# Performance work log

Measured on AMD Instinct MI355X. Metric: run time of the kernel, lower is better.

The kernel has to match this reference:

```python
import jax, jax.numpy as jnp
import numpy as np

B, T, Rn, D, O, E, H, C, TM = 20, 20, 20, 4096, 16, 512, 8, 68, 1900


def l2norm(x, axis=-1, eps=1e-12):
    return x / jnp.maximum(jnp.linalg.norm(x, axis=axis, keepdims=True), eps)


def setup_inputs() -> dict:
    key = jax.random.key(0)
    ks = jax.random.split(key, 10)
    return {
        "features": jax.random.normal(ks[0], (B, T, Rn, D), jnp.float32),
        "labels": jax.random.randint(ks[1], (B, O), 0, C),
        "temporal_mem": jax.random.normal(ks[2], (TM, T, D), jnp.float32),
        "entity_W": jax.random.normal(ks[3], (C, E), jnp.float32) / np.float32(np.sqrt(C)),
        "entity_b": jnp.zeros((E,), jnp.float32),
        "Wq": jax.random.normal(ks[4], (E, E), jnp.float32) / np.float32(np.sqrt(E)),
        "Wk": jax.random.normal(ks[5], (D, E), jnp.float32) / np.float32(np.sqrt(D)),
        "Wv": jax.random.normal(ks[6], (D, E), jnp.float32) / np.float32(np.sqrt(D)),
        "Wo": jax.random.normal(ks[7], (E, E), jnp.float32) / np.float32(np.sqrt(E)),
        "obj_W1": jax.random.normal(ks[8], (D, E), jnp.float32) / np.float32(np.sqrt(D)),
        "obj_b1": jnp.zeros((E,), jnp.float32),
        "obj_W2": jax.random.normal(ks[9], (E, 1), jnp.float32) / np.float32(np.sqrt(E)),
        "obj_b2": jnp.zeros((1,), jnp.float32),
    }


def reference(features, labels, temporal_mem, entity_W, entity_b, Wq, Wk, Wv, Wo,
              obj_W1, obj_b1, obj_W2, obj_b2):
    beta = 0.5   # loss mixing weight (module's beta)
    qgce = 0.7   # generalized-CE exponent
    Dh = E // H
    # region features, L2-normalized (dataset_feat == 'CVPR' path)
    Rf = l2norm(features)                                   # [B,T,Rn,D]

    # ---- temporal memory-bank kNN retrieval ----
    R_max = l2norm(jnp.max(Rf, axis=2))                     # [B,T,D] max-pool over regions
    mem_max = l2norm(jnp.max(temporal_mem, axis=1))         # [TM,D] max-pool over frames
    sim = jnp.einsum('btd,md->btm', R_max, mem_max)         # [B,T,TM]
    idx = jnp.argmax(sim, axis=-1)                          # [B,T] nearest memory slot
    Rp = temporal_mem[idx]                                  # [B,T,T,D] gathered memory videos
    mem_feat = jnp.max(Rp, axis=2)                          # [B,T,D]

    # ---- entity (object-label) embedding: one-hot with class 0 zeroed ----
    onehot = jax.nn.one_hot(labels, C, dtype=features.dtype)
    onehot = onehot * (labels != 0)[..., None].astype(features.dtype)
    Qe = onehot @ entity_W + entity_b                       # [B,O,E]

    # ---- multi-head attention fusion over regions + retrieved memory ----
    kv = jnp.concatenate([Rf.reshape(B, T * Rn, D), mem_feat], axis=1)  # [B,N,D]
    q = (Qe @ Wq).reshape(B, O, H, Dh)
    k = (kv @ Wk).reshape(B, -1, H, Dh)
    v = (kv @ Wv).reshape(B, -1, H, Dh)
    scores = jnp.einsum('bohd,bnhd->bhon', q, k) / np.float32(np.sqrt(Dh))
    attn = jax.nn.softmax(scores, axis=-1)
    fused = jnp.einsum('bhon,bnhd->bohd', attn, v).reshape(B, O, E) @ Wo  # [B,O,E]

    # ---- top-k region objectness selection + generalized CE ----
    QR = jax.lax.stop_gradient(jnp.mean(scores, axis=1)[:, :, :T * Rn].reshape(B, O, T, Rn))
    hi = jnp.argmax(QR, axis=-1)                            # [B,O,T] top-1 region
    lo = jnp.argmin(QR, axis=-1)                            # [B,O,T] low region
    bidx = jnp.arange(B)[:, None, None]
    tidx = jnp.arange(T)[None, None, :]
    R_high = Rf[bidx, tidx, hi]                             # [B,O,T,D]
    R_low = Rf[bidx, tidx, lo]                              # [B,O,T,D]
    osel = (labels != 0).astype(features.dtype)             # [B,O]
    onum = jnp.maximum(jnp.sum(osel, axis=1), 1.0)
    mlp = lambda x: jax.nn.sigmoid(jnp.tanh(x @ obj_W1 + obj_b1) @ obj_W2 + obj_b2)
    s_hi = mlp(R_high * osel[..., None, None]).squeeze(-1)  # [B,O,T]
    s_lo = mlp(R_low * osel[..., None, None]).squeeze(-1)
    gce_hi = jnp.mean((1.0 - (s_hi + 1e-7) ** qgce) / qgce * osel[..., None], axis=-1)
    gce_lo = jnp.mean((1.0 - (1.0 - s_lo + 1e-7) ** qgce) / qgce * osel[..., None], axis=-1)
    gce = jnp.mean(jnp.sum(gce_hi, axis=1) / onum) + jnp.mean(jnp.sum(gce_lo, axis=1) / onum)

    return fused + beta * gce
```

## Files before the change

### kernel.cpp

```cpp
#include <hip/hip_runtime.h>

#define B_   20
#define T_   20
#define RN   20
#define D_   4096
#define O_   16
#define E_   512
#define H_   8
#define DH   64
#define TM_  1900
#define MREG 8192
#define NW   1536
#define NSIM 2048
#define MSIM 512
#define CAP  256

using f32x4  = __attribute__((ext_vector_type(4))) float;
using bf16x8 = __attribute__((ext_vector_type(8))) __bf16;

__device__ __forceinline__ unsigned short f2bf(float f){
  unsigned u = __float_as_uint(f);
  u += 0x7fffu + ((u >> 16) & 1u);
  return (unsigned short)(u >> 16);
}

__device__ __forceinline__ void st_bf4(unsigned short* dst, float4 v){
  ushort4 o = make_ushort4(f2bf(v.x), f2bf(v.y), f2bf(v.z), f2bf(v.w));
  *(ushort4*)dst = o;
}

__device__ __forceinline__ float bsum256(float v, float* sh){
  int t = threadIdx.x;
  for (int o = 32; o; o >>= 1) v += __shfl_down(v, o, 64);
  __syncthreads();
  if ((t & 63) == 0) sh[t >> 6] = v;
  __syncthreads();
  return sh[0] + sh[1] + sh[2] + sh[3];
}

__device__ __forceinline__ float bmax256(float v, float* sh){
  int t = threadIdx.x;
  for (int o = 32; o; o >>= 1) v = fmaxf(v, __shfl_down(v, o, 64));
  __syncthreads();
  if ((t & 63) == 0) sh[t >> 6] = v;
  __syncthreads();
  return fmaxf(fmaxf(sh[0], sh[1]), fmaxf(sh[2], sh[3]));
}

__device__ __forceinline__ void gld16(const void* g, void* l){
  __builtin_amdgcn_global_load_lds(
      (const __attribute__((address_space(1))) unsigned int*)g,
      (__attribute__((address_space(3))) unsigned int*)l, 16, 0, 0);
}

__global__ __launch_bounds__(256) void k_pre(
    const float* __restrict__ F, const float* __restrict__ TMm,
    const float* __restrict__ Wk, const float* __restrict__ Wv, const float* __restrict__ W1,
    unsigned short* __restrict__ Wall,
    unsigned short* __restrict__ A, float* __restrict__ rmaxr, float* __restrict__ rmsum,
    unsigned short* __restrict__ ubf,
    float* __restrict__ umax, float* __restrict__ msum, unsigned short* __restrict__ wnorm,
    unsigned short* __restrict__ gbf,
    const int* __restrict__ labels, const float* __restrict__ entW, const float* __restrict__ entB,
    const float* __restrict__ Wq, float* __restrict__ q){
  __shared__ char smem[4352];
  int bid = blockIdx.x, t = threadIdx.x;
  if (bid < 2048){
    int m = bid;
    if (m >= TM_){
      int4 zz = make_int4(0,0,0,0);
      int4* r1 = (int4*)(wnorm + (size_t)m*D_);
      int4* r2 = (int4*)(gbf + (size_t)m*D_);
      r1[t] = zz; r1[t + 256] = zz;
      r2[t] = zz; r2[t + 256] = zz;
      return;
    }
    float* sh = (float*)smem;
    const float* base = TMm + (size_t)m*T_*D_;
    float4 mx[4];
#pragma unroll
    for (int i = 0; i < 4; ++i) mx[i] = make_float4(-1e30f,-1e30f,-1e30f,-1e30f);
    for (int f = 0; f < T_; ++f){
#pragma unroll
      for (int i = 0; i < 4; ++i){
        float4 v = *(const float4*)(base + (size_t)f*D_ + i*1024 + t*4);
        mx[i].x = fmaxf(mx[i].x, v.x); mx[i].y = fmaxf(mx[i].y, v.y);
        mx[i].z = fmaxf(mx[i].z, v.z); mx[i].w = fmaxf(mx[i].w, v.w);
      }
    }
    float s = 0.f;
#pragma unroll
    for (int i = 0; i < 4; ++i){
      *(float4*)(umax + (size_t)m*D_ + i*1024 + t*4) = mx[i];
      st_bf4(gbf + (size_t)m*D_ + i*1024 + t*4, mx[i]);
      s += mx[i].x*mx[i].x + mx[i].y*mx[i].y + mx[i].z*mx[i].z + mx[i].w*mx[i].w;
    }
    s = bsum256(s, sh);
    if (t == 0) msum[m] = s;
    float inv = 1.f / fmaxf(sqrtf(s), 1e-12f);
#pragma unroll
    for (int i = 0; i < 4; ++i){
      float4 u = mx[i];
      u.x *= inv; u.y *= inv; u.z *= inv; u.w *= inv;
      st_bf4(wnorm + (size_t)m*D_ + i*1024 + t*4, u);
    }
  } else if (bid < 2560){
    int bt = bid - 2048;
    if (bt >= 400){
      int4 zz = make_int4(0,0,0,0);
      int4* r1 = (int4*)(ubf + (size_t)bt*D_);
      r1[t] = zz; r1[t + 256] = zz;
      int base = 8000 + (bt - 400)*2;
#pragma unroll
      for (int k = 0; k < 2; ++k){
        if (base + k < MREG){
          int4* r2 = (int4*)(A + (size_t)(base + k)*D_);
          r2[t] = zz; r2[t + 256] = zz;
        }
      }
      return;
    }
    float* sh = (float*)smem;
    const float* fb = F + (size_t)bt*RN*D_;
    unsigned short* ab = A + (size_t)bt*RN*D_;
    float4 mx[4];
#pragma unroll
    for (int i = 0; i < 4; ++i) mx[i] = make_float4(-1e30f,-1e30f,-1e30f,-1e30f);
    float4 vn[4];
#pragma unroll
    for (int i = 0; i < 4; ++i) vn[i] = *(const float4*)(fb + i*1024 + t*4);
    for (int r = 0; r < RN; ++r){
      float4 v[4];
      float s = 0.f;
#pragma unroll
      for (int i = 0; i < 4; ++i){
        v[i] = vn[i];
        s += v[i].x*v[i].x + v[i].y*v[i].y + v[i].z*v[i].z + v[i].w*v[i].w;
      }
      if (r + 1 < RN){
#pragma unroll
        for (int i = 0; i < 4; ++i)
          vn[i] = *(const float4*)(fb + (size_t)(r+1)*D_ + i*1024 + t*4);
      }
      s = bsum256(s, sh);
      float ri = 1.f / fmaxf(sqrtf(s), 1e-12f);
#pragma unroll
      for (int i = 0; i < 4; ++i){
        v[i].x *= ri; v[i].y *= ri; v[i].z *= ri; v[i].w *= ri;
        st_bf4(ab + (size_t)r*D_ + i*1024 + t*4, v[i]);
        mx[i].x = fmaxf(mx[i].x, v[i].x); mx[i].y = fmaxf(mx[i].y, v[i].y);
        mx[i].z = fmaxf(mx[i].z, v[i].z); mx[i].w = fmaxf(mx[i].w, v[i].w);
      }
    }
    float s2 = 0.f;
#pragma unroll
    for (int i = 0; i < 4; ++i){
      *(float4*)(rmaxr + (size_t)bt*D_ + i*1024 + t*4) = mx[i];
      s2 += mx[i].x*mx[i].x + mx[i].y*mx[i].y + mx[i].z*mx[i].z + mx[i].w*mx[i].w;
    }
    s2 = bsum256(s2, sh);
    if (t == 0) rmsum[bt] = s2;
    float inv = 1.f / fmaxf(sqrtf(s2), 1e-12f);
#pragma unroll
    for (int i = 0; i < 4; ++i){
      float4 u = mx[i];
      u.x *= inv; u.y *= inv; u.z *= inv; u.w *= inv;
      st_bf4(ubf + (size_t)bt*D_ + i*1024 + t*4, u);
    }
  } else if (bid < 8704){
    int wti = bid - 2560;
    float* tile = (float*)smem;
    int kb = (wti & 127) * 32, nb = (wti >> 7) * 32;
    const float* src; int nc0;
    if (nb < 512)      { src = Wk; nc0 = nb; }
    else if (nb < 1024){ src = Wv; nc0 = nb - 512; }
    else               { src = W1; nc0 = nb - 1024; }
    int tx = t & 31, ty = t >> 5;
#pragma unroll
    for (int j = 0; j < 4; ++j){
      int k = kb + ty + j*8;
      tile[(ty + j*8)*33 + tx] = src[(size_t)k*E_ + nc0 + tx];
    }
    __syncthreads();
#pragma unroll
    for (int j = 0; j < 4; ++j){
      int n = nb + ty + j*8;
      int k = kb + tx;
      Wall[(size_t)n*D_ + k] = f2bf(tile[tx*33 + ty + j*8]);
    }
  } else {
    int bo = bid - 8704;
    float* qe = (float*)smem;
    int lab = labels[bo];
    float sel = (lab != 0) ? 1.f : 0.f;
    qe[t]       = sel * entW[(size_t)lab*E_ + t]       + entB[t];
    qe[t + 256] = sel * entW[(size_t)lab*E_ + t + 256] + entB[t + 256];
    __syncthreads();
    float a0 = 0.f, a1 = 0.f;
    for (int ep = 0; ep < E_; ++ep){
      float r = qe[ep];
      a0 += r * Wq[(size_t)ep*E_ + t];
      a1 += r * Wq[(size_t)ep*E_ + t + 256];
    }
    q[(size_t)bo*E_ + t] = a0;
    q[(size_t)bo*E_ + t + 256] = a1;
  }
}

__global__ __launch_bounds__(512, 1) void k_gemm3(
    const unsigned short* __restrict__ Akv, const unsigned short* __restrict__ Wall,
    const unsigned short* __restrict__ ubf, const unsigned short* __restrict__ wnorm,
    const unsigned short* __restrict__ gbf,
    float* __restrict__ C2, float* __restrict__ simc, float* __restrict__ Gc){
  __shared__ char lds[131072];
  int bid = blockIdx.x;
  bid = (bid & 7)*32 + (bid >> 3);
  const unsigned short *A, *Bw; float* C; int nNt, ldc, mt, nt;
  if (bid < 192){       A = Akv; Bw = Wall;  C = C2;   nNt = 6; ldc = NW;   mt = bid/6;  nt = bid%6; }
  else if (bid < 208){  int s = bid - 192;
                        A = ubf; Bw = wnorm; C = simc; nNt = 8; ldc = NSIM; mt = s/8;    nt = s%8; }
  else {                int s = bid - 208;
                        A = gbf; Bw = Wall;  C = Gc;   nNt = 6; ldc = NW;   mt = s/6;    nt = s%6; }
  int tid = threadIdx.x, wid = tid >> 6, l = tid & 63;
  int wr = (wid >> 2) * 128;
  int wc = (wid & 3) * 64;
  int fr = l & 15, fq = l >> 4;
  const char* Ab = (const char*)A + (size_t)mt*256*(size_t)(D_*2);
  const char* Bb = (const char*)Bw + (size_t)nt*256*(size_t)(D_*2);
  f32x4 acc[8][4];
#pragma unroll
  for (int m = 0; m < 8; ++m)
#pragma unroll
    for (int n = 0; n < 4; ++n) acc[m][n] = (f32x4){0.f,0.f,0.f,0.f};

#pragma unroll
  for (int i = 0; i < 4; ++i){
    int idx = i*512 + tid;
    int row = idx >> 3, u = idx & 7;
    int ul = u ^ (row & 7);
    gld16(Ab + (size_t)row*(D_*2) + (size_t)(ul*16), lds + idx*16);
    gld16(Bb + (size_t)row*(D_*2) + (size_t)(ul*16), lds + 32768 + idx*16);
  }
  __syncthreads();

  int c = 0;
  for (int kt = 0; kt < D_/64; ++kt){
    if (kt < D_/64 - 1){
      int ktoff = (kt + 1) * 128;
      char* dA = lds + (c^1)*65536;
      char* dB = dA + 32768;
#pragma unroll
      for (int i = 0; i < 4; ++i){
        int idx = i*512 + tid;
        int row = idx >> 3, u = idx & 7;
        int ul = u ^ (row & 7);
        gld16(Ab + (size_t)row*(D_*2) + ktoff + ul*16, dA + idx*16);
        gld16(Bb + (size_t)row*(D_*2) + ktoff + ul*16, dB + idx*16);
      }
    }
    const char* LA = lds + c*65536;
    const char* LB = LA + 32768;
    bf16x8 bv[4][2];
#pragma unroll
    for (int n = 0; n < 4; ++n)
#pragma unroll
      for (int kk = 0; kk < 2; ++kk){
        int row = wc + n*16 + fr;
        int u = (kk*4 + fq) ^ (row & 7);
        bv[n][kk] = *(const bf16x8*)(LB + row*128 + u*16);
      }
    __builtin_amdgcn_s_setprio(1);
#pragma unroll
    for (int mp = 0; mp < 4; ++mp){
      bf16x8 av[2][2];
#pragma unroll
      for (int mm = 0; mm < 2; ++mm)
#pragma unroll
        for (int kk = 0; kk < 2; ++kk){
          int row = wr + (mp*2 + mm)*16 + fr;
          int u = (kk*4 + fq) ^ (row & 7);
          av[mm][kk] = *(const bf16x8*)(LA + row*128 + u*16);
        }
#pragma unroll
      for (int mm = 0; mm < 2; ++mm)
#pragma unroll
        for (int n = 0; n < 4; ++n)
#pragma unroll
          for (int kk = 0; kk < 2; ++kk)
            acc[mp*2 + mm][n] = __builtin_amdgcn_mfma_f32_16x16x32_bf16(
                av[mm][kk], bv[n][kk], acc[mp*2 + mm][n], 0, 0, 0);
    }
    __builtin_amdgcn_s_setprio(0);
    __syncthreads();
    c ^= 1;
  }
  size_t crow0 = (size_t)mt*256 + wr, ccol0 = (size_t)nt*256 + wc;
#pragma unroll
  for (int m = 0; m < 8; ++m)
#pragma unroll
    for (int n = 0; n < 4; ++n){
      size_t r0 = crow0 + m*16 + fq*4, c0 = ccol0 + n*16 + fr;
#pragma unroll
      for (int j = 0; j < 4; ++j)
        C[(r0 + j)*(size_t)ldc + c0] = acc[m][n][j];
    }
}

__global__ __launch_bounds__(256) void k_pick(const float* __restrict__ simc,
                                              const float* __restrict__ rmaxr, const float* __restrict__ rmsum,
                                              const float* __restrict__ umax, const float* __restrict__ msum,
                                              const float* __restrict__ Gc, float* __restrict__ C2){
  int bt = blockIdx.x, t = threadIdx.x;
  __shared__ float srow[1920];
  __shared__ float sh[4];
  __shared__ int cnt;
  __shared__ int cl[CAP];
  for (int m = t; m < TM_; m += 256) srow[m] = simc[(size_t)bt*NSIM + m];
  if (t == 0) cnt = 0;
  __syncthreads();
  float mx = -1e30f;
  for (int m = t; m < TM_; m += 256) mx = fmaxf(mx, srow[m]);
  mx = bmax256(mx, sh);
  float thr = mx - 2.5e-4f;
  for (int m = t; m < TM_; m += 256){
    if (srow[m] >= thr){
      int p = atomicAdd(&cnt, 1);
      if (p < CAP) cl[p] = m;
    }
  }
  __syncthreads();
  int cn = cnt < CAP ? cnt : CAP;
  float rinvv = 1.f / fmaxf(sqrtf(rmsum[bt]), 1e-12f);
  const float* a = rmaxr + (size_t)bt*D_;
  float best = -1e30f; int bestm = 0x7fffffff;
  for (int ci = 0; ci < cn; ++ci){
    int m = cl[ci];
    const float* wrow = umax + (size_t)m*D_;
    float p = 0.f;
    for (int i = t*4; i < D_; i += 1024){
      float4 av = *(const float4*)(a + i);
      float4 wv = *(const float4*)(wrow + i);
      p += av.x*wv.x + av.y*wv.y + av.z*wv.z + av.w*wv.w;
    }
    p = bsum256(p, sh);
    float sim = p * rinvv * (1.f / fmaxf(sqrtf(msum[m]), 1e-12f));
    if (sim > best || (sim == best && m < bestm)){ best = sim; bestm = m; }
  }
  const float4* src = (const float4*)(Gc + (size_t)bestm*NW);
  float4* dst = (float4*)(C2 + (size_t)(MREG + bt)*NW);
  if (t < 128){ dst[t] = src[t]; dst[t + 128] = src[t + 128]; dst[t + 256] = src[t + 256]; }
}

__global__ __launch_bounds__(256) void k_post(const float* __restrict__ q, const float* __restrict__ c2,
                                              float* __restrict__ fpre, int* __restrict__ hi,
                                              int* __restrict__ lo, const float* __restrict__ b1,
                                              const float* __restrict__ W2, const float* __restrict__ b2,
                                              float* __restrict__ z){
  __shared__ char smem[58368];
  int bid = blockIdx.x, t = threadIdx.x;
  if (bid < 160){
    int b = bid >> 3, h = bid & 7;
    int w = t >> 6, l = t & 63;
    float* qhp = (float*)smem;
    float* kb  = (float*)(smem + 4160);
    float* sc  = (float*)(smem + 31460);
    for (int i = t; i < O_*DH; i += 256){
      int o = i >> 6, d = i & 63;
      qhp[o*65 + d] = q[((size_t)(b*O_ + o))*E_ + h*DH + d] * 0.125f;
    }
    __syncthreads();
    for (int c = 0; c < 4; ++c){
      for (int i = t; i < 105*DH; i += 256){
        int j = i >> 6, d = i & 63;
        int n = c*105 + j;
        size_t row = n < 400 ? (size_t)b*400 + n : (size_t)MREG + b*20 + (n - 400);
        kb[j*65 + d] = c2[row*NW + h*DH + d];
      }
      __syncthreads();
      for (int i = t; i < O_*105; i += 256){
        int o = i / 105, j = i % 105;
        float acc = 0.f;
        for (int d = 0; d < DH; ++d) acc += qhp[o*65 + d] * kb[j*65 + d];
        sc[o*420 + c*105 + j] = acc;
      }
      __syncthreads();
    }
    for (int oi = 0; oi < 4; ++oi){
      int o = w + oi*4;
      float mxv = -1e30f;
      for (int n = l; n < 420; n += 64) mxv = fmaxf(mxv, sc[o*420 + n]);
      for (int of = 32; of; of >>= 1) mxv = fmaxf(mxv, __shfl_xor(mxv, of, 64));
      float sum = 0.f;
      for (int n = l; n < 420; n += 64){ float e = expf(sc[o*420 + n] - mxv); sc[o*420 + n] = e; sum += e; }
      for (int of = 32; of; of >>= 1) sum += __shfl_xor(sum, of, 64);
      float inv = 1.f / sum;
      for (int n = l; n < 420; n += 64) sc[o*420 + n] *= inv;
    }
    __syncthreads();
    float acc[4] = {0.f, 0.f, 0.f, 0.f};
    for (int c = 0; c < 4; ++c){
      for (int i = t; i < 105*DH; i += 256){
        int j = i >> 6, d = i & 63;
        int n = c*105 + j;
        size_t row = n < 400 ? (size_t)b*400 + n : (size_t)MREG + b*20 + (n - 400);
        kb[j*65 + d] = c2[row*NW + E_ + h*DH + d];
      }
      __syncthreads();
#pragma unroll
      for (int og = 0; og < 4; ++og){
        int o = og*4 + w;
        float a = 0.f;
        for (int j = 0; j < 105; ++j) a += sc[o*420 + c*105 + j] * kb[j*65 + l];
        acc[og] += a;
      }
      __syncthreads();
    }
#pragma unroll
    for (int og = 0; og < 4; ++og){
      int o = og*4 + w;
      fpre[((size_t)(b*O_ + o))*E_ + h*DH + l] = acc[og];
    }
  } else if (bid < 560){
    int bt = bid - 160;
    int b = bt / T_, tt = bt % T_;
    float* kl = (float*)smem;
    float* qr = (float*)(smem + 41040);
    for (int i = t; i < RN*E_; i += 256){
      int r = i >> 9, e = i & 511;
      kl[r*513 + e] = c2[((size_t)b*400 + tt*RN + r)*NW + e];
    }
    __syncthreads();
#pragma unroll
    for (int pp = 0; pp < 2; ++pp){
      int p = t + pp*256;
      if (p < O_*RN){
        int o = p / RN, r = p % RN;
        const float* qrow = q + ((size_t)(b*O_ + o))*E_;
        float acc = 0.f;
        for (int e = 0; e < E_; ++e) acc += qrow[e] * kl[r*513 + e];
        qr[o*20 + r] = acc;
      }
    }
    __syncthreads();
    if (t < O_){
      int o = t;
      float bh = qr[o*20], bl = qr[o*20]; int ih = 0, il = 0;
#pragma unroll
      for (int r = 1; r < RN; ++r){
        float v = qr[o*20 + r];
        if (v > bh){ bh = v; ih = r; }
        if (v < bl){ bl = v; il = r; }
      }
      int rowbase = b*400 + tt*RN;
      int outi = (b*O_ + o)*T_ + tt;
      hi[outi] = rowbase + ih;
      lo[outi] = rowbase + il;
    }
  } else {
    int g = (bid - 560)*4 + (t >> 6);
    int l = t & 63;
    const float* hrow = c2 + (size_t)g*NW + 1024;
    float acc = 0.f;
    for (int e = l; e < E_; e += 64) acc += tanhf(hrow[e] + b1[e]) * W2[e];
    for (int of = 32; of; of >>= 1) acc += __shfl_down(acc, of, 64);
    if (l == 0) z[g] = 1.f / (1.f + expf(-(acc + b2[0])));
  }
}

__global__ __launch_bounds__(256) void k_outg(const float* __restrict__ fpre, const float* __restrict__ Wo,
                                              const float* __restrict__ z, const int* __restrict__ hi,
                                              const int* __restrict__ lo, const int* __restrict__ labels,
                                              float* __restrict__ out){
  int bo = blockIdx.x, t = threadIdx.x;
  __shared__ float rowv[E_];
  __shared__ float vb[B_];
  __shared__ int cb[B_];
  __shared__ float gsh;
  rowv[t] = fpre[(size_t)bo*E_ + t];
  rowv[t + 256] = fpre[(size_t)bo*E_ + t + 256];
  if (t < B_){ vb[t] = 0.f; cb[t] = 0; }
  __syncthreads();
  for (int p = t; p < B_*O_; p += 256){
    int b = p / O_;
    if (labels[p] != 0){
      float acc = 0.f;
      for (int tt = 0; tt < T_; ++tt){
        float shi = z[hi[p*T_ + tt]];
        float slo = z[lo[p*T_ + tt]];
        acc += (1.f - __powf(shi + 1e-7f, 0.7f)) / 0.7f;
        acc += (1.f - __powf(1.f - slo + 1e-7f, 0.7f)) / 0.7f;
      }
      atomicAdd(&vb[b], acc / (float)T_);
      atomicAdd(&cb[b], 1);
    }
  }
  __syncthreads();
  if (t == 0){
    float g = 0.f;
    for (int b = 0; b < B_; ++b) g += vb[b] / fmaxf((float)cb[b], 1.f);
    gsh = 0.5f * (g / (float)B_);
  }
  __syncthreads();
  float g = gsh;
  float a0 = 0.f, a1 = 0.f;
  for (int ep = 0; ep < E_; ++ep){
    float r = rowv[ep];
    a0 += r * Wo[(size_t)ep*E_ + t];
    a1 += r * Wo[(size_t)ep*E_ + t + 256];
  }
  out[(size_t)bo*E_ + t] = a0 + g;
  out[(size_t)bo*E_ + t + 256] = a1 + g;
}

extern "C" void kernel_launch(void* const* d_in, const int* in_sizes, int n_in,
                              void* d_out, int out_size, void* d_ws, size_t ws_size,
                              hipStream_t stream) {
  (void)in_sizes; (void)n_in; (void)out_size; (void)ws_size;
  const float* F    = (const float*)d_in[0];
  const int*   labels = (const int*)d_in[1];
  const float* TMm  = (const float*)d_in[2];
  const float* entW = (const float*)d_in[3];
  const float* entB = (const float*)d_in[4];
  const float* Wq   = (const float*)d_in[5];
  const float* Wk   = (const float*)d_in[6];
  const float* Wv   = (const float*)d_in[7];
  const float* Wo   = (const float*)d_in[8];
  const float* W1   = (const float*)d_in[9];
  const float* b1   = (const float*)d_in[10];
  const float* W2   = (const float*)d_in[11];
  const float* b2   = (const float*)d_in[12];
  float* out = (float*)d_out;

  size_t off = 0;
  char* wsb = (char*)d_ws;
  auto alloc = [&](size_t bytes) -> char* {
    char* p = wsb + off; off += (bytes + 255) & ~(size_t)255; return p;
  };
  unsigned short* A_kv = (unsigned short*)alloc((size_t)MREG * D_ * 2);
  unsigned short* Wall = (unsigned short*)alloc((size_t)NW * D_ * 2);
  float* umax          = (float*)alloc((size_t)TM_ * D_ * 4);
  unsigned short* gbf  = (unsigned short*)alloc((size_t)NSIM * D_ * 2);
  unsigned short* wnorm= (unsigned short*)alloc((size_t)NSIM * D_ * 2);
  unsigned short* ubf  = (unsigned short*)alloc((size_t)MSIM * D_ * 2);
  float* rmaxr = (float*)alloc((size_t)400 * D_ * 4);
  float* simc  = (float*)alloc((size_t)MSIM * NSIM * 4);
  float* Gc    = (float*)alloc((size_t)NSIM * NW * 4);
  float* C2    = (float*)alloc((size_t)(MREG + 512) * NW * 4);
  float* qbuf  = (float*)alloc((size_t)B_ * O_ * E_ * 4);
  float* fpre  = (float*)alloc((size_t)B_ * O_ * E_ * 4);
  float* rmsum = (float*)alloc(400 * 4);
  float* msum  = (float*)alloc(TM_ * 4);
  int*   hib   = (int*)alloc(6400 * 4);
  int*   lob   = (int*)alloc(6400 * 4);
  float* zbuf  = (float*)alloc(8000 * 4);

  k_pre<<<9024, 256, 0, stream>>>(F, TMm, Wk, Wv, W1, Wall, A_kv, rmaxr, rmsum, ubf,
                                  umax, msum, wnorm, gbf, labels, entW, entB, Wq, qbuf);
  k_gemm3<<<256, 512, 0, stream>>>(A_kv, Wall, ubf, wnorm, gbf, C2, simc, Gc);
  k_pick<<<400, 256, 0, stream>>>(simc, rmaxr, rmsum, umax, msum, Gc, C2);
  k_post<<<2560, 256, 0, stream>>>(qbuf, C2, fpre, hib, lob, b1, W2, b2, zbuf);
  k_outg<<<B_*O_, 256, 0, stream>>>(fpre, Wo, zbuf, hib, lob, labels, out);
}
```

Baseline: 485.9 us.

## Use triple-buffered K=32 LDS pipeline in GEMM and prefetch frames in max-pool

The main GEMM kernel moves from a double-buffered K=64 tile with full __syncthreads to a three-stage K=32 ring buffer. It uses explicit vmcnt waits and raw s_barrier so two tiles of global loads stay in flight while MFMAs run on the third. The LDS footprint drops from 128 KiB to 96 KiB and the swizzle changes to 4 chunks per row. The memory max-pool loop also double-buffers its frame loads in registers to hide load latency. The hand-written vmcnt counts depend on exactly four outstanding loads per stage, so any compiler reordering of those loads could make the waits insufficient.

```diff
diff --git a/kernel.cpp b/kernel.cpp
--- a/kernel.cpp
+++ b/kernel.cpp
@@ -14,6 +14,7 @@
 #define NSIM 2048
 #define MSIM 512
 #define CAP  256
+#define NT32 128
 
 using f32x4  = __attribute__((ext_vector_type(4))) float;
 using bf16x8 = __attribute__((ext_vector_type(8))) __bf16;
@@ -80,12 +81,21 @@
     float4 mx[4];
 #pragma unroll
     for (int i = 0; i < 4; ++i) mx[i] = make_float4(-1e30f,-1e30f,-1e30f,-1e30f);
+    float4 va[2][4];
+#pragma unroll
+    for (int i = 0; i < 4; ++i) va[0][i] = *(const float4*)(base + i*1024 + t*4);
+#pragma unroll
     for (int f = 0; f < T_; ++f){
+      int c = f & 1;
+      if (f + 1 < T_){
+#pragma unroll
+        for (int i = 0; i < 4; ++i)
+          va[c^1][i] = *(const float4*)(base + (size_t)(f+1)*D_ + i*1024 + t*4);
+      }
 #pragma unroll
       for (int i = 0; i < 4; ++i){
-        float4 v = *(const float4*)(base + (size_t)f*D_ + i*1024 + t*4);
-        mx[i].x = fmaxf(mx[i].x, v.x); mx[i].y = fmaxf(mx[i].y, v.y);
-        mx[i].z = fmaxf(mx[i].z, v.z); mx[i].w = fmaxf(mx[i].w, v.w);
+        mx[i].x = fmaxf(mx[i].x, va[c][i].x); mx[i].y = fmaxf(mx[i].y, va[c][i].y);
+        mx[i].z = fmaxf(mx[i].z, va[c][i].z); mx[i].w = fmaxf(mx[i].w, va[c][i].w);
       }
     }
     float s = 0.f;
@@ -212,7 +222,7 @@
     const unsigned short* __restrict__ ubf, const unsigned short* __restrict__ wnorm,
     const unsigned short* __restrict__ gbf,
     float* __restrict__ C2, float* __restrict__ simc, float* __restrict__ Gc){
-  __shared__ char lds[131072];
+  __shared__ char lds[98304];
   int bid = blockIdx.x;
   bid = (bid & 7)*32 + (bid >> 3);
   const unsigned short *A, *Bw; float* C; int nNt, ldc, mt, nt;
@@ -233,66 +243,60 @@
 #pragma unroll
     for (int n = 0; n < 4; ++n) acc[m][n] = (f32x4){0.f,0.f,0.f,0.f};
 
-#pragma unroll
-  for (int i = 0; i < 4; ++i){
-    int idx = i*512 + tid;
-    int row = idx >> 3, u = idx & 7;
-    int ul = u ^ (row & 7);
-    gld16(Ab + (size_t)row*(D_*2) + (size_t)(ul*16), lds + idx*16);
-    gld16(Bb + (size_t)row*(D_*2) + (size_t)(ul*16), lds + 32768 + idx*16);
-  }
-  __syncthreads();
-
-  int c = 0;
-  for (int kt = 0; kt < D_/64; ++kt){
-    if (kt < D_/64 - 1){
-      int ktoff = (kt + 1) * 128;
-      char* dA = lds + (c^1)*65536;
-      char* dB = dA + 32768;
-#pragma unroll
-      for (int i = 0; i < 4; ++i){
-        int idx = i*512 + tid;
-        int row = idx >> 3, u = idx & 7;
-        int ul = u ^ (row & 7);
-        gld16(Ab + (size_t)row*(D_*2) + ktoff + ul*16, dA + idx*16);
-        gld16(Bb + (size_t)row*(D_*2) + ktoff + ul*16, dB + idx*16);
-      }
-    }
-    const char* LA = lds + c*65536;
-    const char* LB = LA + 32768;
-    bf16x8 bv[4][2];
-#pragma unroll
-    for (int n = 0; n < 4; ++n)
-#pragma unroll
-      for (int kk = 0; kk < 2; ++kk){
-        int row = wc + n*16 + fr;
-        int u = (kk*4 + fq) ^ (row & 7);
-        bv[n][kk] = *(const bf16x8*)(LB + row*128 + u*16);
-      }
+  auto stage = [&](char* dst, int ktt){
+    int ktoff = ktt * 64;
+#pragma unroll
+    for (int i = 0; i < 2; ++i){
+      int s = i*512 + tid;
+      int row = s >> 2, u = s & 3;
+      int ul = u ^ (row & 3);
+      gld16(Ab + (size_t)row*(D_*2) + ktoff + ul*16, dst + s*16);
+      gld16(Bb + (size_t)row*(D_*2) + ktoff + ul*16, dst + 16384 + s*16);
+    }
+  };
+
+  stage(lds, 0);
+  stage(lds + 32768, 1);
+  stage(lds + 65536, 2);
+
+  int cur = 0;
+  for (int kt = 0; kt < NT32; ++kt){
+    if (kt < NT32 - 2)       asm volatile("s_waitcnt vmcnt(8)" ::: "memory");
+    else if (kt == NT32 - 2) asm volatile("s_waitcnt vmcnt(4)" ::: "memory");
+    else                     asm volatile("s_waitcnt vmcnt(0)" ::: "memory");
+    __builtin_amdgcn_s_barrier();
+    __builtin_amdgcn_sched_barrier(0);
+    const char* LA = lds + cur*32768;
+    const char* LB = LA + 16384;
+    bf16x8 bv[4];
+#pragma unroll
+    for (int n = 0; n < 4; ++n){
+      int row = wc + n*16 + fr;
+      int u = fq ^ (row & 3);
+      bv[n] = *(const bf16x8*)(LB + row*64 + u*16);
+    }
     __builtin_amdgcn_s_setprio(1);
 #pragma unroll
     for (int mp = 0; mp < 4; ++mp){
-      bf16x8 av[2][2];
+      bf16x8 av[2];
+#pragma unroll
+      for (int mm = 0; mm < 2; ++mm){
+        int row = wr + (mp*2 + mm)*16 + fr;
+        int u = fq ^ (row & 3);
+        av[mm] = *(const bf16x8*)(LA + row*64 + u*16);
+      }
 #pragma unroll
       for (int mm = 0; mm < 2; ++mm)
 #pragma unroll
-        for (int kk = 0; kk < 2; ++kk){
-          int row = wr + (mp*2 + mm)*16 + fr;
-          int u = (kk*4 + fq) ^ (row & 7);
-          av[mm][kk] = *(const bf16x8*)(LA + row*128 + u*16);
-        }
-#pragma unroll
-      for (int mm = 0; mm < 2; ++mm)
-#pragma unroll
         for (int n = 0; n < 4; ++n)
-#pragma unroll
-          for (int kk = 0; kk < 2; ++kk)
-            acc[mp*2 + mm][n] = __builtin_amdgcn_mfma_f32_16x16x32_bf16(
-                av[mm][kk], bv[n][kk], acc[mp*2 + mm][n], 0, 0, 0);
+          acc[mp*2 + mm][n] = __builtin_amdgcn_mfma_f32_16x16x32_bf16(
+              av[mm], bv[n], acc[mp*2 + mm][n], 0, 0, 0);
     }
     __builtin_amdgcn_s_setprio(0);
-    __syncthreads();
-    c ^= 1;
+    __builtin_amdgcn_s_barrier();
+    if (kt + 3 < NT32)
+      stage(lds + cur*32768, kt + 3);
+    cur = (cur == 2) ? 0 : cur + 1;
   }
   size_t crow0 = (size_t)mt*256 + wr, ccol0 = (size_t)nt*256 + wc;
 #pragma unroll
```

After: 514.7 us. 1.06x slower.
